# Performance work log

Measured on AMD Instinct MI355X. Metric: run time of the kernel, lower is better.

The kernel has to match this reference:

```python
import jax, jax.numpy as jnp
import numpy as np

NUM_NODES = 2
ALPHA = 1.0
BETA = 5.0
KL_BETA = 1.0
LOG_2PI = float(np.log(2.0 * np.pi))

K_COMP = 8192   # number of KDE components / empirical samples
N_SAMP = 8192   # n_samples drawn from the KDE
B_X = 2048      # x_data batch
D_W = NUM_NODES * NUM_NODES + 4 * NUM_NODES + 1  # 13 weights per sample


def setup_inputs() -> dict:
    key = jax.random.key(0)
    k1, k2, k3, k4, k5 = jax.random.split(key, 5)
    return {
        "emp_samples": jax.random.normal(k1, (K_COMP, D_W), dtype=jnp.float32),
        "log_kde_rhos": jnp.zeros((K_COMP,), dtype=jnp.float32),
        "x": jax.random.normal(k2, (B_X, 1), dtype=jnp.float32),
        "y": jax.random.normal(k3, (B_X,), dtype=jnp.float32),
        "eps": jax.random.normal(k4, (N_SAMP, D_W), dtype=jnp.float32),
        "rand_idxs": jax.random.randint(k5, (N_SAMP,), 0, K_COMP, dtype=jnp.int64 if jax.config.jax_enable_x64 else jnp.int32),
    }


def _batch_regression(w, x):
    # w: [N, 13], x: [B, 1] -> y_preds [N, B]
    n = NUM_NODES
    i = 0
    w1 = w[:, i:i + n]; i += n                                   # [N, n]
    b1 = w[:, i:i + n]; i += n                                   # [N, n]
    w2 = w[:, i:i + n * n].reshape(-1, n, n); i += n * n         # [N, n, n]
    b2 = w[:, i:i + n]; i += n                                   # [N, n]
    w3 = w[:, i:i + n]; i += n                                   # [N, n]
    b3 = w[:, i]                                                 # [N]
    h = jnp.einsum('bi,kj->bki', w1, x) + b1[:, None, :]         # [N, B, n]
    h = jnp.tanh(h)
    h = jnp.einsum('bij,bkj->bki', w2, h) + b2[:, None, :]
    h = jnp.tanh(h)
    return jnp.einsum('bi,bki->bk', w3, h) + b3[:, None]         # [N, B]


def reference(emp_samples, log_kde_rhos, x, y, eps, rand_idxs):
    kde_std = jax.nn.softplus(log_kde_rhos)                      # [K]
    kde_var = kde_std * kde_std                                  # [K]
    # sample_from_kde (noise externalized)
    w = emp_samples[rand_idxs] + eps * kde_std[rand_idxs][:, None]  # [N, D]
    # data likelihood: Normal(y_pred, 1/sqrt(beta))
    y_preds = _batch_regression(w, x)                            # [N, B]
    ll = -0.5 * BETA * (y_preds - y[None, :]) ** 2 + 0.5 * (jnp.log(BETA) - LOG_2PI)
    data_lp = ll.sum(-1).mean()
    # weight prior: Normal(0, 1/sqrt(alpha)), sum over weight dim
    prior_lp = (-0.5 * ALPHA * w * w + 0.5 * (jnp.log(ALPHA) - LOG_2PI)).sum(1)  # [N]
    # KDE mixture log-prob: isotropic Gaussian components, uniform weights
    d = w.shape[1]
    sq = (jnp.sum(w * w, axis=1)[:, None]
          - 2.0 * (w @ emp_samples.T)
          + jnp.sum(emp_samples * emp_samples, axis=1)[None, :])  # [N, K]
    comp_lp = -0.5 * (d * LOG_2PI + d * jnp.log(kde_var)[None, :] + sq / kde_var[None, :])
    q_lp = jax.scipy.special.logsumexp(comp_lp, axis=1) - jnp.log(jnp.float32(emp_samples.shape[0]))  # [N]
    kl_term = (q_lp - prior_lp).mean()
    return data_lp - KL_BETA * kl_term
```

## Files before the change

kernel.cpp:

```cpp
#include <hip/hip_runtime.h>
#include <math.h>

#define KCOMP 8192
#define NSAMP 8192
#define BX 2048
#define DW 13

#define LOG2PI  1.8378770664093453f
#define LOGBETA 1.6094379124341003f
#define LOGK    9.0109131020929380f
#define LOG2E   1.4426950408889634f
#define LN2     0.6931471805599453f
#define C2E     2.8853900817779268f

#define NBLK_KL   1024
#define NBLK_DATA 2048
#define NBLK_MONO (NBLK_KL + NBLK_DATA)

#define NK     512
#define XLO    (-4.75f)
#define DXK    (9.5f / (float)NK)
#define USCALE ((float)NK / 9.5f)

typedef __attribute__((ext_vector_type(8))) short bf16x8_t;
typedef __attribute__((ext_vector_type(4))) float f32x4_t;

__device__ __forceinline__ float fast_log(float x) {
    return __builtin_amdgcn_logf(x) * LN2;
}
__device__ __forceinline__ float softplus_stable(float x) {
    return fmaxf(x, 0.0f) + log1pf(expf(-fabsf(x)));
}
__device__ __forceinline__ unsigned short to_bf16(float f) {
    unsigned int u = __builtin_bit_cast(unsigned int, f);
    u += 0x7FFFu + ((u >> 16) & 1u);
    return (unsigned short)(u >> 16);
}
__device__ __forceinline__ float from_bf16(unsigned short h) {
    unsigned int u = ((unsigned int)h) << 16;
    return __builtin_bit_cast(float, u);
}
__device__ __forceinline__ void tanh_pair(float a0, float a1, float& t0, float& t1) {
    float e0 = __builtin_amdgcn_exp2f(a0);
    float e1 = __builtin_amdgcn_exp2f(a1);
    float d0 = e0 + 1.0f, d1 = e1 + 1.0f;
    float inv = __builtin_amdgcn_rcpf(d0 * d1);
    t0 = fmaf(-2.0f, d1 * inv, 1.0f);
    t1 = fmaf(-2.0f, d0 * inv, 1.0f);
}

#define OFF_PART  0
#define OFF_RSUM  2048
#define OFF_G2    10240
#define OFF_A2    18432
#define OFF_HQ    26624
#define OFF_PL    34816
#define OFF_WF    43008
#define OFF_WB    174080
#define OFF_EMPB  305152

__global__ __launch_bounds__(256) void prep_kernel(
        const float* __restrict__ emp, const float* __restrict__ rhos,
        const float* __restrict__ eps, const int* __restrict__ idxs,
        float* __restrict__ ws) {
    int g = blockIdx.x * 256 + threadIdx.x;
    if (g < KCOMP) {
        int j = g;
        ws[OFF_RSUM + j] = 0.0f;
        unsigned short* empB = (unsigned short*)(ws + OFF_EMPB);
        float sp  = softplus_stable(rhos[j]);
        float var = sp * sp;
        float inv = 1.0f / var;
        float esq = 0.0f;
        #pragma unroll
        for (int c = 0; c < DW; ++c) {
            float e = emp[j * DW + c];
            esq = fmaf(e, e, esq);
            unsigned short eb = to_bf16(e);
            empB[j * 32 + c]      = eb;
            empB[j * 32 + 16 + c] = eb;
        }
        #pragma unroll
        for (int c = DW; c < 16; ++c) { empB[j*32+c] = 0; empB[j*32+16+c] = 0; }
        float f1v = -6.5f * (LOG2PI + logf(var)) - 0.5f * esq * inv;
        ws[OFF_G2 + j] = inv * LOG2E;
        ws[OFF_A2 + j] = f1v * LOG2E;
    } else {
        int b  = g - KCOMP;
        int i0 = idxs[b];
        unsigned short* wB = (unsigned short*)(ws + OFF_WB);
        float* wF = ws + OFF_WF;
        float sp  = softplus_stable(rhos[i0]);
        float var = sp * sp;
        float inv = 1.0f / var;
        float esq = 0.0f, wsq = 0.0f, dot = 0.0f;
        #pragma unroll
        for (int c = 0; c < DW; ++c) {
            float e  = emp[i0 * DW + c];
            float wc = fmaf(eps[b * DW + c], sp, e);
            esq = fmaf(e, e, esq);
            wsq = fmaf(wc, wc, wsq);
            dot = fmaf(wc, e, dot);
            wF[b * 16 + c] = wc;
            unsigned short hi = to_bf16(wc);
            wB[b * 32 + c]      = hi;
            wB[b * 32 + 16 + c] = to_bf16(wc - from_bf16(hi));
        }
        #pragma unroll
        for (int c = DW; c < 16; ++c) { wF[b*16+c] = 0.0f; wB[b*32+c] = 0; wB[b*32+16+c] = 0; }
        float f1v = -6.5f * (LOG2PI + logf(var)) - 0.5f * esq * inv;
        float h   = 0.5f * wsq;
        ws[OFF_HQ + b] = h;
        ws[OFF_PL + b] = fmaf(inv, dot - h, f1v) * LOG2E;
    }
}

__global__ __launch_bounds__(256) void main_kernel(
        float* __restrict__ ws, const float* __restrict__ x,
        const float* __restrict__ y) {
    __shared__ float kn[4][NK + 1];
    __shared__ float red[4];
    int tid = threadIdx.x, wave = tid >> 6, lane = tid & 63;

    float* part = ws + OFF_PART;
    float* rsum = ws + OFF_RSUM;
    const float* G2  = ws + OFF_G2;
    const float* A2  = ws + OFF_A2;
    const float* hqA = ws + OFF_HQ;
    const float* plA = ws + OFF_PL;
    const float* wF  = ws + OFF_WF;
    const unsigned short* wB   = (const unsigned short*)(ws + OFF_WB);
    const unsigned short* empB = (const unsigned short*)(ws + OFF_EMPB);

    if (blockIdx.x >= NBLK_KL) {
        int b = (blockIdx.x - NBLK_KL) * 4 + wave;
        float w[DW];
        #pragma unroll
        for (int c = 0; c < DW; ++c) w[c] = wF[b * 16 + c];
        float s0 = w[0]*C2E, s1 = w[1]*C2E, s2 = w[2]*C2E, s3 = w[3]*C2E;
        float s4 = w[4]*C2E, s5 = w[5]*C2E, s6 = w[6]*C2E, s7 = w[7]*C2E;
        float s8 = w[8]*C2E, s9 = w[9]*C2E;

        float* knw = kn[wave];
        #pragma unroll
        for (int kk = 0; kk < NK / 64 + 1; ++kk) {
            int idx = kk * 64 + lane;
            if (idx <= NK) {
                float xk = fmaf((float)idx, DXK, XLO);
                float h10, h11, h20, h21;
                tanh_pair(fmaf(s0, xk, s2), fmaf(s1, xk, s3), h10, h11);
                tanh_pair(fmaf(s4, h10, fmaf(s5, h11, s8)),
                          fmaf(s6, h10, fmaf(s7, h11, s9)), h20, h21);
                knw[idx] = fmaf(w[10], h20, fmaf(w[11], h21, w[12]));
            }
        }
        __syncthreads();

        const float4* x4 = (const float4*)x;
        const float4* y4 = (const float4*)y;
        float acc = 0.0f;
        for (int it = 0; it < BX / 4 / 128; ++it) {
            int k0 = it * 128 + lane;
            float4 tva = x4[k0];
            float4 tvb = x4[k0 + 64];
            float4 yva = y4[k0];
            float4 yvb = y4[k0 + 64];
            float tt[8] = {tva.x, tva.y, tva.z, tva.w, tvb.x, tvb.y, tvb.z, tvb.w};
            float yy[8] = {yva.x, yva.y, yva.z, yva.w, yvb.x, yvb.y, yvb.z, yvb.w};
            #pragma unroll
            for (int p = 0; p < 8; ++p) {
                float u = fmaf(tt[p], USCALE, (float)(NK / 2));
                u = fminf(fmaxf(u, 0.0f), (float)NK - 0.001f);
                int   i = (int)u;
                float f = u - (float)i;
                float k0v = knw[i];
                float k1v = knw[i + 1];
                float yp  = fmaf(f, k1v - k0v, k0v);
                float d   = yp - yy[p];
                acc = fmaf(d, d, acc);
            }
        }
        #pragma unroll
        for (int o = 32; o; o >>= 1) acc += __shfl_down(acc, o);
        if (lane == 0) red[wave] = acc;
        __syncthreads();
        if (tid == 0) part[blockIdx.x - NBLK_KL] = red[0] + red[1] + red[2] + red[3];
    } else {
        int bid     = blockIdx.x;
        int rowtile = bid & 127;
        int chunk   = bid >> 7;
        int rowbase = rowtile * 64 + wave * 16;
        int half = lane >> 4;
        int m16  = lane & 15;

        const bf16x8_t afrag = *(const bf16x8_t*)(wB + (rowbase + m16) * 32 + half * 8);
        float h[4], p[4];
        #pragma unroll
        for (int r = 0; r < 4; ++r) {
            h[r] = hqA[rowbase + half * 4 + r];
            p[r] = plA[rowbase + half * 4 + r];
        }
        float s[4] = {0.f, 0.f, 0.f, 0.f};

        int j0 = chunk * (KCOMP / 8);
        #pragma unroll 2
        for (int jt = 0; jt < (KCOMP / 8) / 16; ++jt) {
            int j = j0 + jt * 16 + m16;
            bf16x8_t bfrag = *(const bf16x8_t*)(empB + j * 32 + half * 8);
            f32x4_t c = {0.f, 0.f, 0.f, 0.f};
            c = __builtin_amdgcn_mfma_f32_16x16x32_bf16(afrag, bfrag, c, 0, 0, 0);
            float g2 = G2[j], a2 = A2[j];
            #pragma unroll
            for (int r = 0; r < 4; ++r) {
                float t = fmaf(-g2, h[r], a2 - p[r]);
                s[r] += __builtin_amdgcn_exp2f(fmaf(g2, c[r], t));
            }
        }
        #pragma unroll
        for (int r = 0; r < 4; ++r) {
            float S = s[r];
            S += __shfl_xor(S, 1); S += __shfl_xor(S, 2);
            S += __shfl_xor(S, 4); S += __shfl_xor(S, 8);
            if (m16 == 0) atomicAdd(&rsum[rowbase + half * 4 + r], S);
        }
    }
}

__global__ __launch_bounds__(1024) void fin_kernel(
        const float* __restrict__ ws, float* __restrict__ out) {
    __shared__ float red1[16], red2[16];
    int tid = threadIdx.x, wave = tid >> 6, lane = tid & 63;

    const float* part = ws + OFF_PART;
    const float* rsum = ws + OFF_RSUM;
    const float* hqA  = ws + OFF_HQ;
    const float* plA  = ws + OFF_PL;

    float s1 = 0.0f;
    for (int i = tid; i < NBLK_DATA; i += 1024) s1 += part[i];
    float s2 = 0.0f;
    for (int b = tid; b < NSAMP; b += 1024) {
        float q     = plA[b] * LN2 + fast_log(rsum[b]) - LOGK;
        float prior = -hqA[b] - 6.5f * LOG2PI;
        s2 += q - prior;
    }
    #pragma unroll
    for (int o = 32; o; o >>= 1) { s1 += __shfl_down(s1, o); s2 += __shfl_down(s2, o); }
    if (lane == 0) { red1[wave] = s1; red2[wave] = s2; }
    __syncthreads();
    if (tid < 16) {
        s1 = red1[tid]; s2 = red2[tid];
        #pragma unroll
        for (int o = 8; o; o >>= 1) { s1 += __shfl_down(s1, o); s2 += __shfl_down(s2, o); }
        if (tid == 0) {
            float data_lp = -2.5f * s1 / (float)NSAMP
                            + (float)BX * 0.5f * (LOGBETA - LOG2PI);
            out[0] = data_lp - s2 / (float)NSAMP;
        }
    }
}

extern "C" void kernel_launch(void* const* d_in, const int* in_sizes, int n_in,
                              void* d_out, int out_size, void* d_ws, size_t ws_size,
                              hipStream_t stream) {
    const float* emp  = (const float*)d_in[0];
    const float* rhos = (const float*)d_in[1];
    const float* x    = (const float*)d_in[2];
    const float* y    = (const float*)d_in[3];
    const float* eps  = (const float*)d_in[4];
    const int*   idxs = (const int*)d_in[5];
    float* out = (float*)d_out;
    float* ws  = (float*)d_ws;

    prep_kernel<<<64, 256, 0, stream>>>(emp, rhos, eps, idxs, ws);
    main_kernel<<<NBLK_MONO, 256, 0, stream>>>(ws, x, y);
    fin_kernel<<<1, 1024, 0, stream>>>(ws, out);
}
```

Measured before the change: 99.08 us.

## Process four samples per wave in data-likelihood blocks to amortize x/y loads

```diff
diff --git a/kernel.cpp b/kernel.cpp
--- a/kernel.cpp
+++ b/kernel.cpp
@@ -14,10 +14,11 @@
 #define C2E     2.8853900817779268f
 
 #define NBLK_KL   1024
-#define NBLK_DATA 2048
+#define NBLK_DATA 512
 #define NBLK_MONO (NBLK_KL + NBLK_DATA)
 
 #define NK     512
+#define KSTR   520
 #define XLO    (-4.75f)
 #define DXK    (9.5f / (float)NK)
 #define USCALE ((float)NK / 9.5f)
@@ -118,7 +119,7 @@
 __global__ __launch_bounds__(256) void main_kernel(
         float* __restrict__ ws, const float* __restrict__ x,
         const float* __restrict__ y) {
-    __shared__ float kn[4][NK + 1];
+    __shared__ float kn[16 * KSTR];
     __shared__ float red[4];
     int tid = threadIdx.x, wave = tid >> 6, lane = tid & 63;
 
@@ -133,29 +134,33 @@
     const unsigned short* empB = (const unsigned short*)(ws + OFF_EMPB);
 
     if (blockIdx.x >= NBLK_KL) {
-        int b = (blockIdx.x - NBLK_KL) * 4 + wave;
-        float w[DW];
-        #pragma unroll
-        for (int c = 0; c < DW; ++c) w[c] = wF[b * 16 + c];
-        float s0 = w[0]*C2E, s1 = w[1]*C2E, s2 = w[2]*C2E, s3 = w[3]*C2E;
-        float s4 = w[4]*C2E, s5 = w[5]*C2E, s6 = w[6]*C2E, s7 = w[7]*C2E;
-        float s8 = w[8]*C2E, s9 = w[9]*C2E;
-
-        float* knw = kn[wave];
-        #pragma unroll
-        for (int kk = 0; kk < NK / 64 + 1; ++kk) {
-            int idx = kk * 64 + lane;
-            if (idx <= NK) {
+        int d = blockIdx.x - NBLK_KL;
+
+        {
+            int t   = tid >> 4;
+            int sub = tid & 15;
+            int row = d * 16 + t;
+            float wv[DW];
+            #pragma unroll
+            for (int c = 0; c < DW; ++c) wv[c] = wF[row * 16 + c];
+            float s0 = wv[0]*C2E, s1 = wv[1]*C2E, s2 = wv[2]*C2E, s3 = wv[3]*C2E;
+            float s4 = wv[4]*C2E, s5 = wv[5]*C2E, s6 = wv[6]*C2E, s7 = wv[7]*C2E;
+            float s8 = wv[8]*C2E, s9 = wv[9]*C2E;
+            for (int idx = sub; idx <= NK; idx += 16) {
                 float xk = fmaf((float)idx, DXK, XLO);
                 float h10, h11, h20, h21;
                 tanh_pair(fmaf(s0, xk, s2), fmaf(s1, xk, s3), h10, h11);
                 tanh_pair(fmaf(s4, h10, fmaf(s5, h11, s8)),
                           fmaf(s6, h10, fmaf(s7, h11, s9)), h20, h21);
-                knw[idx] = fmaf(w[10], h20, fmaf(w[11], h21, w[12]));
+                kn[t * KSTR + idx] = fmaf(wv[10], h20, fmaf(wv[11], h21, wv[12]));
             }
         }
         __syncthreads();
 
+        const float* tb0 = kn + (wave * 4 + 0) * KSTR;
+        const float* tb1 = kn + (wave * 4 + 1) * KSTR;
+        const float* tb2 = kn + (wave * 4 + 2) * KSTR;
+        const float* tb3 = kn + (wave * 4 + 3) * KSTR;
         const float4* x4 = (const float4*)x;
         const float4* y4 = (const float4*)y;
         float acc = 0.0f;
@@ -173,18 +178,25 @@
                 u = fminf(fmaxf(u, 0.0f), (float)NK - 0.001f);
                 int   i = (int)u;
                 float f = u - (float)i;
-                float k0v = knw[i];
-                float k1v = knw[i + 1];
-                float yp  = fmaf(f, k1v - k0v, k0v);
-                float d   = yp - yy[p];
-                acc = fmaf(d, d, acc);
+                float a0 = tb0[i], b0 = tb0[i + 1];
+                float a1 = tb1[i], b1 = tb1[i + 1];
+                float a2 = tb2[i], b2 = tb2[i + 1];
+                float a3 = tb3[i], b3 = tb3[i + 1];
+                float d0 = fmaf(f, b0 - a0, a0) - yy[p];
+                float d1 = fmaf(f, b1 - a1, a1) - yy[p];
+                float d2 = fmaf(f, b2 - a2, a2) - yy[p];
+                float d3 = fmaf(f, b3 - a3, a3) - yy[p];
+                acc = fmaf(d0, d0, acc);
+                acc = fmaf(d1, d1, acc);
+                acc = fmaf(d2, d2, acc);
+                acc = fmaf(d3, d3, acc);
             }
         }
         #pragma unroll
         for (int o = 32; o; o >>= 1) acc += __shfl_down(acc, o);
         if (lane == 0) red[wave] = acc;
         __syncthreads();
-        if (tid == 0) part[blockIdx.x - NBLK_KL] = red[0] + red[1] + red[2] + red[3];
+        if (tid == 0) part[d] = red[0] + red[1] + red[2] + red[3];
     } else {
         int bid     = blockIdx.x;
         int rowtile = bid & 127;
```

Measured after the change: 107.8 us. 1.09x slower.
